# Performance work log

Measured on AMD Instinct MI355X. Metric: run time of the kernel, lower is better.

Reference implementation:

```python
import jax, jax.numpy as jnp
import numpy as np

S = 2   # scale_factor
K = 5   # k_up
M = 48  # m_channels
KE = 3  # k_encoder


def conv2d(x, w, b, pad):
    # NCHW conv, stride 1, symmetric padding (matches nn.Conv2d(padding=pad))
    y = jax.lax.conv_general_dilated(
        x, w, window_strides=(1, 1), padding=[(pad, pad), (pad, pad)],
        dimension_numbers=("NCHW", "OIHW", "NCHW"))
    return y + b[None, :, None, None]


def setup_inputs() -> dict:
    key = jax.random.key(0)
    k1, k2, k3, k4, k5 = jax.random.split(key, 5)
    C_in = 64
    x = jax.random.normal(k1, (8, C_in, 128, 128), dtype=jnp.float32)
    w_compress = jax.random.normal(k2, (M, C_in, 1, 1), dtype=jnp.float32) * 0.1
    b_compress = jax.random.normal(k3, (M,), dtype=jnp.float32) * 0.05
    w_encoder = jax.random.normal(k4, ((K * S) ** 2, M, KE, KE), dtype=jnp.float32) * 0.05
    b_encoder = jax.random.normal(k5, ((K * S) ** 2,), dtype=jnp.float32) * 0.05
    return {"x": x, "w_compress": w_compress, "b_compress": b_compress,
            "w_encoder": w_encoder, "b_encoder": b_encoder}


def reference(x, w_compress, b_compress, w_encoder, b_encoder):
    B, C, H, W = x.shape
    # mask branch: compress -> relu -> encoder -> softmax over k_up^2
    y = jax.nn.relu(conv2d(x, w_compress, b_compress, pad=0))
    y = conv2d(y, w_encoder, b_encoder, pad=KE // 2)          # [B, (K*S)^2, H, W]
    y = y.reshape(B, S * S, K * K, H, W)
    y = jax.nn.softmax(y, axis=2)
    # unfold x with kernel K, pad K//2, stride 1 -> [B, C, K*K, H, W]
    p = K // 2
    xpad = jnp.pad(x, ((0, 0), (0, 0), (p, p), (p, p)))
    unf = jnp.stack([xpad[:, :, i:i + H, j:j + W]
                     for i in range(K) for j in range(K)], axis=2)
    # per-subpixel softmax-weighted patch sum; channel layout (scale_idx, C)
    out = jnp.einsum("bskhw,bckhw->bschw", y, unf)            # [B, S^2, C, H, W]
    out = out.reshape(B, S * S * C, H, W)
    # PixelShuffle(S): view (B, C_out, r, r, H, W) -> (B, C_out, H, r, W, r)
    r = S
    c_out = (S * S * C) // (r * r)
    out = out.reshape(B, c_out, r, r, H, W).transpose(0, 1, 4, 2, 5, 3)
    return out.reshape(B, c_out, H * r, W * r)
```

## Files before the change

### kernel.cpp

```cpp
#include <hip/hip_runtime.h>

#define HW 16384

typedef __bf16 bf16x8 __attribute__((ext_vector_type(8)));
typedef __bf16 bf16x4 __attribute__((ext_vector_type(4)));
typedef float  f32x4  __attribute__((ext_vector_type(4)));
typedef float  f32x2  __attribute__((ext_vector_type(2)));

__global__ __launch_bounds__(256)
void prep_w(const float* __restrict__ we, const float* __restrict__ wc,
            __bf16* __restrict__ wt, __bf16* __restrict__ wcb) {
    int idx = blockIdx.x * 256 + threadIdx.x;
    if (idx < 128 * 448) {
        int e = idx / 448, k = idx % 448;
        float v = 0.f;
        if (e < 100 && k < 432) {
            int t = k / 48, m = k % 48;
            v = we[(e * 48 + m) * 9 + t];
        }
        wt[idx] = (__bf16)v;
    } else {
        idx -= 128 * 448;
        if (idx < 48 * 64) wcb[idx] = (__bf16)wc[idx];
    }
}

__global__ __launch_bounds__(256, 2)
void prep_xty1(const float* __restrict__ x, const __bf16* __restrict__ wcb,
               const float* __restrict__ bc,
               __bf16* __restrict__ xt, __bf16* __restrict__ y1o) {
    __shared__ __align__(16) float lds[256 * 65];
    __bf16* y1s = (__bf16*)lds;

    const int b = blockIdx.x & 7, chunk = blockIdx.x >> 3;
    const int t = threadIdx.x;
    const int lane = t & 63, wv = t >> 6;
    const int lgp = lane >> 4, lr = lane & 15;
    const int pos0 = chunk * 256;

    const float* xb = x + (size_t)b * 64 * HW + pos0;
    for (int c = 0; c < 64; ++c)
        lds[t * 65 + c] = xb[(size_t)c * HW + t];
    __syncthreads();

    {
        const int q = t & 3, pp = t >> 2;
        #pragma unroll
        for (int it = 0; it < 4; ++it) {
            int pos = it * 64 + pp;
            __bf16* o = xt + ((size_t)b * HW + pos0 + pos) * 64 + q * 16;
            bf16x8 v0, v1;
            #pragma unroll
            for (int e = 0; e < 8; ++e) {
                v0[e] = (__bf16)lds[pos * 65 + q * 16 + e];
                v1[e] = (__bf16)lds[pos * 65 + q * 16 + 8 + e];
            }
            *(bf16x8*)o       = v0;
            *(bf16x8*)(o + 8) = v1;
        }
    }
    bf16x8 af[4][2];
    #pragma unroll
    for (int i = 0; i < 4; ++i) {
        int pix = (wv * 4 + i) * 16 + lr;
        #pragma unroll
        for (int kc = 0; kc < 2; ++kc)
            #pragma unroll
            for (int e = 0; e < 8; ++e)
                af[i][kc][e] = (__bf16)lds[pix * 65 + kc * 32 + lgp * 8 + e];
    }
    __syncthreads();

    {
        bf16x8 bw[3][2];
        f32x4 bias4[3];
        #pragma unroll
        for (int nt = 0; nt < 3; ++nt) {
            bias4[nt] = *(const f32x4*)(bc + nt * 16 + lgp * 4);
            #pragma unroll
            for (int kc = 0; kc < 2; ++kc)
                bw[nt][kc] = *(const bf16x8*)(wcb + (nt * 16 + lr) * 64 + kc * 32 + lgp * 8);
        }
        #pragma unroll
        for (int i = 0; i < 4; ++i) {
            int pix = (wv * 4 + i) * 16 + lr;
            #pragma unroll
            for (int nt = 0; nt < 3; ++nt) {
                f32x4 cc = bias4[nt];
                cc = __builtin_amdgcn_mfma_f32_16x16x32_bf16(bw[nt][0], af[i][0], cc, 0, 0, 0);
                cc = __builtin_amdgcn_mfma_f32_16x16x32_bf16(bw[nt][1], af[i][1], cc, 0, 0, 0);
                bf16x4 o4;
                #pragma unroll
                for (int r = 0; r < 4; ++r) o4[r] = (__bf16)fmaxf(cc[r], 0.f);
                *(bf16x4*)(y1s + pix * 56 + nt * 16 + lgp * 4) = o4;
            }
        }
    }
    __syncthreads();

    __bf16* yo = y1o + (size_t)(b * HW + pos0) * 48;
    #pragma unroll
    for (int i = 0; i < 6; ++i) {
        int c = i * 256 + t;
        int pix = (c * 10923) >> 16;
        int mc  = c - pix * 6;
        bf16x8 v = *(bf16x8*)(y1s + pix * 56 + mc * 8);
        *(bf16x8*)(yo + (size_t)c * 8) = v;
    }
}

__global__ __launch_bounds__(256, 2)
void carafe_weights(const __bf16* __restrict__ y1g,
                    const __bf16* __restrict__ wt, const float* __restrict__ be,
                    unsigned int* __restrict__ wnp) {
    __shared__ __align__(16) char smem[59392];
    __bf16*    y1  = (__bf16*)smem;
    _Float16*  lgt = (_Float16*)smem;

    const int tid = threadIdx.x;
    const int lane = tid & 63, wv = tid >> 6;
    const int lgp = lane >> 4, lr = lane & 15;
    const int b = blockIdx.x & 7, tile = blockIdx.x >> 3;
    const int h0 = (tile >> 3) << 4, w0 = (tile & 7) << 4;

    const __bf16* y1b = y1g + (size_t)b * HW * 48;
    #pragma unroll
    for (int it = 0; it < 8; ++it) {
        int id = it * 256 + tid;
        if (id < 1944) {
            int hr  = (id * 607) >> 16;
            int rem = id - hr * 108;
            int wc  = (rem * 10923) >> 16;
            int mc  = rem - wc * 6;
            int hy = h0 - 1 + hr, wx = w0 - 1 + wc;
            bf16x8 v = {};
            if (hy >= 0 && hy < 128 && wx >= 0 && wx < 128)
                v = *(const bf16x8*)(y1b + (size_t)(hy * 128 + wx) * 48 + mc * 8);
            *(bf16x8*)(y1 + (hr * 18 + wc) * 56 + mc * 8) = v;
        }
    }
    for (int i = tid; i < 1120; i += 256)
        y1[324 * 56 + i] = (__bf16)0.f;
    __syncthreads();

    f32x4 acc[4][7];
    #pragma unroll
    for (int ot = 0; ot < 7; ++ot) {
        int o_ = ot * 16 + lr;
        float bz = (o_ < 100) ? be[o_] : 0.f;
        #pragma unroll
        for (int i = 0; i < 4; ++i) acc[i][ot] = {bz, bz, bz, bz};
    }
    const int ptg0 = wv * 4;

    auto ldA = [&](bf16x8 A[4], int kc) {
        int Kb = kc * 32 + lgp * 8;
        int t  = (Kb * 683) >> 15;  int m0 = Kb - t * 48;
        int ty = (t * 11) >> 5;     int tx = t - ty * 3;
        int base = ty * 18 + lr + tx;
        #pragma unroll
        for (int i = 0; i < 4; ++i)
            A[i] = *(const bf16x8*)(y1 + ((ptg0 + i) * 18 + base) * 56 + m0);
    };
    auto ldB = [&](bf16x8 B[7], int kc) {
        #pragma unroll
        for (int j = 0; j < 7; ++j)
            B[j] = *(const bf16x8*)(wt + (j * 16 + lr) * 448 + kc * 32 + lgp * 8);
    };
    auto mm = [&](bf16x8 A[4], bf16x8 B[7]) {
        #pragma unroll
        for (int i = 0; i < 4; ++i)
            #pragma unroll
            for (int j = 0; j < 7; ++j)
                acc[i][j] = __builtin_amdgcn_mfma_f32_16x16x32_bf16(A[i], B[j], acc[i][j], 0, 0, 0);
    };

    bf16x8 A0[4], B0[7], A1[4], B1[7];
    ldA(A0, 0); ldB(B0, 0);
    #pragma unroll
    for (int kc = 0; kc < 14; kc += 2) {
        if (kc + 1 < 14) { ldA(A1, kc + 1); ldB(B1, kc + 1); }
        mm(A0, B0);
        if (kc + 2 < 14) { ldA(A0, kc + 2); ldB(B0, kc + 2); }
        if (kc + 1 < 14) mm(A1, B1);
    }
    __syncthreads();

    #pragma unroll
    for (int i = 0; i < 4; ++i)
        #pragma unroll
        for (int j = 0; j < 7; ++j) {
            int o_ = j * 16 + lr;
            #pragma unroll
            for (int r = 0; r < 4; ++r) {
                int p = (ptg0 + i) * 16 + lgp * 4 + r;
                lgt[p * 116 + o_] = (_Float16)acc[i][j][r];
            }
        }
    __syncthreads();

    const _Float16* lrow = lgt + tid * 116;
    #pragma unroll
    for (int s2 = 0; s2 < 2; ++s2) {
        unsigned int* wp = wnp + (size_t)(b * 2 + s2) * 25 * HW + tile * 256 + tid;
        #pragma unroll
        for (int k = 0; k < 25; ++k) {
            unsigned short lo = __builtin_bit_cast(unsigned short, lrow[(2 * s2) * 25 + k]);
            unsigned short hi = __builtin_bit_cast(unsigned short, lrow[(2 * s2 + 1) * 25 + k]);
            wp[(size_t)k * HW] = (unsigned int)lo | ((unsigned int)hi << 16);
        }
    }
}

__global__ __launch_bounds__(512, 2)
void carafe_apply(const __bf16* __restrict__ xt, const unsigned int* __restrict__ wnp,
                  float* __restrict__ out) {
    __shared__ __bf16 lx[400 * 68];

    const int tid = threadIdx.x;
    const int b = blockIdx.x & 7, tile = blockIdx.x >> 3;
    const int h0 = (tile >> 3) << 4, w0 = (tile & 7) << 4;

    const int l8 = tid & 7, pg = tid >> 3;
    bf16x8 hv[7];
    #pragma unroll
    for (int it = 0; it < 7; ++it) {
        int pos = it * 64 + pg;
        bf16x8 v = {};
        if (pos < 400) {
            int r = pos / 20, q = pos % 20;
            int hy = h0 - 2 + r, wx = w0 - 2 + q;
            if (hy >= 0 && hy < 128 && wx >= 0 && wx < 128)
                v = *(const bf16x8*)(xt + ((size_t)b * HW + hy * 128 + wx) * 64 + l8 * 8);
        }
        hv[it] = v;
    }

    const int pix = tid & 255, sgrp = tid >> 8;
    const int py = pix >> 4, px = pix & 15;
    const int h = h0 + py, w = w0 + px;
    float wt_[50];
    {
        const unsigned int* wp = wnp + (size_t)(b * 2 + sgrp) * 25 * HW + tile * 256 + pix;
        #pragma unroll
        for (int k = 0; k < 25; ++k) {
            unsigned int u = wp[(size_t)k * HW];
            wt_[k]      = (float)__builtin_bit_cast(_Float16, (unsigned short)(u & 0xffffu));
            wt_[25 + k] = (float)__builtin_bit_cast(_Float16, (unsigned short)(u >> 16));
        }
        #pragma unroll
        for (int g = 0; g < 2; ++g) {
            float* v = wt_ + g * 25;
            float mx = v[0];
            #pragma unroll
            for (int k = 1; k < 25; ++k) mx = fmaxf(mx, v[k]);
            float s = 0.f;
            #pragma unroll
            for (int k = 0; k < 25; ++k) { v[k] = __expf(v[k] - mx); s += v[k]; }
            float inv = 1.f / s;
            #pragma unroll
            for (int k = 0; k < 25; ++k) v[k] *= inv;
        }
    }

    #pragma unroll
    for (int it = 0; it < 7; ++it) {
        int pos = it * 64 + pg;
        if (pos < 400) {
            bf16x4 vlo = {hv[it][0], hv[it][1], hv[it][2], hv[it][3]};
            bf16x4 vhi = {hv[it][4], hv[it][5], hv[it][6], hv[it][7]};
            *(bf16x4*)(lx + pos * 68 + l8 * 8)     = vlo;
            *(bf16x4*)(lx + pos * 68 + l8 * 8 + 4) = vhi;
        }
    }
    __syncthreads();

    float* ob = out + (size_t)b * 256 * HW;
    #pragma unroll 1
    for (int cq = 0; cq < 16; ++cq) {
        f32x2 a0 = {0.f, 0.f}, a1 = {0.f, 0.f}, a2 = {0.f, 0.f}, a3 = {0.f, 0.f};
        #pragma unroll
        for (int ki = 0; ki < 5; ++ki) {
            const int rowbase = (py + ki) * 20 + px;
            #pragma unroll
            for (int kj = 0; kj < 5; ++kj) {
                uint2 u = *(const uint2*)(lx + (rowbase + kj) * 68 + cq * 4);
                f32x2 xlo = { __uint_as_float(u.x << 16), __uint_as_float(u.x & 0xffff0000u) };
                f32x2 xhi = { __uint_as_float(u.y << 16), __uint_as_float(u.y & 0xffff0000u) };
                float wA = wt_[ki * 5 + kj];
                float wB = wt_[25 + ki * 5 + kj];
                a0 += xlo * wA;
                a1 += xhi * wA;
                a2 += xlo * wB;
                a3 += xhi * wB;
            }
        }
        size_t base0 = ((size_t)(sgrp * 32 + cq) * 256 + 2 * h) * 256 + 2 * w;
        size_t base1 = base0 + (size_t)16 * 256 * 256;
        __builtin_nontemporal_store(a0, (f32x2*)(ob + base0));
        __builtin_nontemporal_store(a1, (f32x2*)(ob + base0 + 256));
        __builtin_nontemporal_store(a2, (f32x2*)(ob + base1));
        __builtin_nontemporal_store(a3, (f32x2*)(ob + base1 + 256));
    }
}

extern "C" void kernel_launch(void* const* d_in, const int* in_sizes, int n_in,
                              void* d_out, int out_size, void* d_ws, size_t ws_size,
                              hipStream_t stream) {
    const float* x  = (const float*)d_in[0];
    const float* wc = (const float*)d_in[1];
    const float* bc = (const float*)d_in[2];
    const float* we = (const float*)d_in[3];
    const float* be = (const float*)d_in[4];
    float* out = (float*)d_out;

    __bf16*       xt  = (__bf16*)d_ws;
    __bf16*       y1g = (__bf16*)((char*)d_ws + 16777216);
    __bf16*       wte = (__bf16*)((char*)d_ws + 41943040);
    __bf16*       wcb = (__bf16*)((char*)d_ws + 41943040 + 114688);
    unsigned int* wnp = (unsigned int*)((char*)d_ws + 41943040 + 114688 + 6144);

    prep_w<<<236, 256, 0, stream>>>(we, wc, wte, wcb);
    prep_xty1<<<512, 256, 0, stream>>>(x, wcb, bc, xt, y1g);
    carafe_weights<<<512, 256, 0, stream>>>(y1g, wte, be, wnp);
    carafe_apply<<<512, 512, 0, stream>>>(xt, wnp, out);
}
```

Measured before the change: 91.96 us.

## Fuse encoder-logit and reassembly kernels, keeping softmax weights in shared memory

```diff
diff --git a/kernel.cpp b/kernel.cpp
--- a/kernel.cpp
+++ b/kernel.cpp
@@ -110,12 +110,13 @@
 }
 
 __global__ __launch_bounds__(256, 2)
-void carafe_weights(const __bf16* __restrict__ y1g,
-                    const __bf16* __restrict__ wt, const float* __restrict__ be,
-                    unsigned int* __restrict__ wnp) {
-    __shared__ __align__(16) char smem[59392];
+void carafe_wa(const __bf16* __restrict__ xt, const __bf16* __restrict__ y1g,
+               const __bf16* __restrict__ wt, const float* __restrict__ be,
+               float* __restrict__ out) {
+    __shared__ __align__(16) char smem[60416];
     __bf16*    y1  = (__bf16*)smem;
     _Float16*  lgt = (_Float16*)smem;
+    __bf16*    lx  = (__bf16*)smem;
 
     const int tid = threadIdx.x;
     const int lane = tid & 63, wv = tid >> 6;
@@ -194,40 +195,17 @@
             #pragma unroll
             for (int r = 0; r < 4; ++r) {
                 int p = (ptg0 + i) * 16 + lgp * 4 + r;
-                lgt[p * 116 + o_] = (_Float16)acc[i][j][r];
+                lgt[p * 118 + o_] = (_Float16)acc[i][j][r];
             }
         }
-    __syncthreads();
-
-    const _Float16* lrow = lgt + tid * 116;
-    #pragma unroll
-    for (int s2 = 0; s2 < 2; ++s2) {
-        unsigned int* wp = wnp + (size_t)(b * 2 + s2) * 25 * HW + tile * 256 + tid;
-        #pragma unroll
-        for (int k = 0; k < 25; ++k) {
-            unsigned short lo = __builtin_bit_cast(unsigned short, lrow[(2 * s2) * 25 + k]);
-            unsigned short hi = __builtin_bit_cast(unsigned short, lrow[(2 * s2 + 1) * 25 + k]);
-            wp[(size_t)k * HW] = (unsigned int)lo | ((unsigned int)hi << 16);
-        }
-    }
-}
-
-__global__ __launch_bounds__(512, 2)
-void carafe_apply(const __bf16* __restrict__ xt, const unsigned int* __restrict__ wnp,
-                  float* __restrict__ out) {
-    __shared__ __bf16 lx[400 * 68];
-
-    const int tid = threadIdx.x;
-    const int b = blockIdx.x & 7, tile = blockIdx.x >> 3;
-    const int h0 = (tile >> 3) << 4, w0 = (tile & 7) << 4;
-
-    const int l8 = tid & 7, pg = tid >> 3;
-    bf16x8 hv[7];
-    #pragma unroll
-    for (int it = 0; it < 7; ++it) {
-        int pos = it * 64 + pg;
+
+    bf16x8 hv[13];
+    #pragma unroll
+    for (int it = 0; it < 13; ++it) {
+        int id = it * 256 + tid;
         bf16x8 v = {};
-        if (pos < 400) {
+        if (id < 3200) {
+            int pos = id >> 3, l8 = id & 7;
             int r = pos / 20, q = pos % 20;
             int hy = h0 - 2 + r, wx = w0 - 2 + q;
             if (hy >= 0 && hy < 128 && wx >= 0 && wx < 128)
@@ -235,22 +213,18 @@
         }
         hv[it] = v;
     }
-
-    const int pix = tid & 255, sgrp = tid >> 8;
-    const int py = pix >> 4, px = pix & 15;
+    __syncthreads();
+
+    const int py = tid >> 4, px = tid & 15;
     const int h = h0 + py, w = w0 + px;
-    float wt_[50];
+    float wt_[100];
     {
-        const unsigned int* wp = wnp + (size_t)(b * 2 + sgrp) * 25 * HW + tile * 256 + pix;
-        #pragma unroll
-        for (int k = 0; k < 25; ++k) {
-            unsigned int u = wp[(size_t)k * HW];
-            wt_[k]      = (float)__builtin_bit_cast(_Float16, (unsigned short)(u & 0xffffu));
-            wt_[25 + k] = (float)__builtin_bit_cast(_Float16, (unsigned short)(u >> 16));
-        }
-        #pragma unroll
-        for (int g = 0; g < 2; ++g) {
+        const _Float16* lrow = lgt + tid * 118;
+        #pragma unroll
+        for (int g = 0; g < 4; ++g) {
             float* v = wt_ + g * 25;
+            #pragma unroll
+            for (int k = 0; k < 25; ++k) v[k] = (float)lrow[g * 25 + k];
             float mx = v[0];
             #pragma unroll
             for (int k = 1; k < 25; ++k) mx = fmaxf(mx, v[k]);
@@ -262,11 +236,13 @@
             for (int k = 0; k < 25; ++k) v[k] *= inv;
         }
     }
-
-    #pragma unroll
-    for (int it = 0; it < 7; ++it) {
-        int pos = it * 64 + pg;
-        if (pos < 400) {
+    __syncthreads();
+
+    #pragma unroll
+    for (int it = 0; it < 13; ++it) {
+        int id = it * 256 + tid;
+        if (id < 3200) {
+            int pos = id >> 3, l8 = id & 7;
             bf16x4 vlo = {hv[it][0], hv[it][1], hv[it][2], hv[it][3]};
             bf16x4 vhi = {hv[it][4], hv[it][5], hv[it][6], hv[it][7]};
             *(bf16x4*)(lx + pos * 68 + l8 * 8)     = vlo;
@@ -278,7 +254,8 @@
     float* ob = out + (size_t)b * 256 * HW;
     #pragma unroll 1
     for (int cq = 0; cq < 16; ++cq) {
-        f32x2 a0 = {0.f, 0.f}, a1 = {0.f, 0.f}, a2 = {0.f, 0.f}, a3 = {0.f, 0.f};
+        f32x2 g0l = {0.f, 0.f}, g0h = {0.f, 0.f}, g1l = {0.f, 0.f}, g1h = {0.f, 0.f};
+        f32x2 g2l = {0.f, 0.f}, g2h = {0.f, 0.f}, g3l = {0.f, 0.f}, g3h = {0.f, 0.f};
         #pragma unroll
         for (int ki = 0; ki < 5; ++ki) {
             const int rowbase = (py + ki) * 20 + px;
@@ -287,20 +264,24 @@
                 uint2 u = *(const uint2*)(lx + (rowbase + kj) * 68 + cq * 4);
                 f32x2 xlo = { __uint_as_float(u.x << 16), __uint_as_float(u.x & 0xffff0000u) };
                 f32x2 xhi = { __uint_as_float(u.y << 16), __uint_as_float(u.y & 0xffff0000u) };
-                float wA = wt_[ki * 5 + kj];
-                float wB = wt_[25 + ki * 5 + kj];
-                a0 += xlo * wA;
-                a1 += xhi * wA;
-                a2 += xlo * wB;
-                a3 += xhi * wB;
+                const int k = ki * 5 + kj;
+                float w0_ = wt_[k], w1_ = wt_[25 + k], w2_ = wt_[50 + k], w3_ = wt_[75 + k];
+                g0l += xlo * w0_;  g0h += xhi * w0_;
+                g1l += xlo * w1_;  g1h += xhi * w1_;
+                g2l += xlo * w2_;  g2h += xhi * w2_;
+                g3l += xlo * w3_;  g3h += xhi * w3_;
             }
         }
-        size_t base0 = ((size_t)(sgrp * 32 + cq) * 256 + 2 * h) * 256 + 2 * w;
-        size_t base1 = base0 + (size_t)16 * 256 * 256;
-        __builtin_nontemporal_store(a0, (f32x2*)(ob + base0));
-        __builtin_nontemporal_store(a1, (f32x2*)(ob + base0 + 256));
-        __builtin_nontemporal_store(a2, (f32x2*)(ob + base1));
-        __builtin_nontemporal_store(a3, (f32x2*)(ob + base1 + 256));
+        const size_t pstride = (size_t)16 * 256 * 256;
+        size_t base = ((size_t)cq * 256 + 2 * h) * 256 + 2 * w;
+        __builtin_nontemporal_store(g0l, (f32x2*)(ob + base));
+        __builtin_nontemporal_store(g0h, (f32x2*)(ob + base + 256));
+        __builtin_nontemporal_store(g1l, (f32x2*)(ob + base + pstride));
+        __builtin_nontemporal_store(g1h, (f32x2*)(ob + base + pstride + 256));
+        __builtin_nontemporal_store(g2l, (f32x2*)(ob + base + 2 * pstride));
+        __builtin_nontemporal_store(g2h, (f32x2*)(ob + base + 2 * pstride + 256));
+        __builtin_nontemporal_store(g3l, (f32x2*)(ob + base + 3 * pstride));
+        __builtin_nontemporal_store(g3h, (f32x2*)(ob + base + 3 * pstride + 256));
     }
 }
 
@@ -314,14 +295,12 @@
     const float* be = (const float*)d_in[4];
     float* out = (float*)d_out;
 
-    __bf16*       xt  = (__bf16*)d_ws;
-    __bf16*       y1g = (__bf16*)((char*)d_ws + 16777216);
-    __bf16*       wte = (__bf16*)((char*)d_ws + 41943040);
-    __bf16*       wcb = (__bf16*)((char*)d_ws + 41943040 + 114688);
-    unsigned int* wnp = (unsigned int*)((char*)d_ws + 41943040 + 114688 + 6144);
+    __bf16* xt  = (__bf16*)d_ws;
+    __bf16* y1g = (__bf16*)((char*)d_ws + 16777216);
+    __bf16* wte = (__bf16*)((char*)d_ws + 41943040);
+    __bf16* wcb = (__bf16*)((char*)d_ws + 41943040 + 114688);
 
     prep_w<<<236, 256, 0, stream>>>(we, wc, wte, wcb);
     prep_xty1<<<512, 256, 0, stream>>>(x, wcb, bc, xt, y1g);
-    carafe_weights<<<512, 256, 0, stream>>>(y1g, wte, be, wnp);
-    carafe_apply<<<512, 512, 0, stream>>>(xt, wnp, out);
+    carafe_wa<<<512, 256, 0, stream>>>(xt, y1g, wte, be, out);
 }
```

Result: faster. 79.69 us, median of 2 (-13.3%).
